# Kernel tuning notes

Measured on AMD Instinct MI355X. Metric: run time of the kernel, lower is better.

Reference implementation:

```python
import jax, jax.numpy as jnp
import numpy as np

B, S, E, H = 2, 2048, 1024, 16
D = E // H          # head_dim = 64
HK = H // 4         # heads per kernel group = 4
MASKED_BIAS = -10000.0


def _dwconv_causal(x, w, b):
    # x: [B, h, S, D], w: [D, k], b: [D]; causal depthwise conv along S
    k = w.shape[1]
    s = x.shape[2]
    xp = jnp.pad(x, ((0, 0), (0, 0), (k - 1, 0), (0, 0)))
    out = b
    for i in range(k):
        out = out + xp[:, :, i:i + s, :] * w[:, i]
    return out


def setup_inputs() -> dict:
    key = jax.random.key(0)
    ks = jax.random.split(key, 32)
    inp = {
        'hidden_states': jax.random.normal(ks[0], (B, S, E), jnp.float32),
        'c_attn_w': jax.random.normal(ks[1], (E, 3 * E), jnp.float32) * 0.02,
        'c_attn_b': jnp.zeros((3 * E,), jnp.float32),
        'c_proj_w': jax.random.normal(ks[2], (E, E), jnp.float32) * 0.02,
        'c_proj_b': jnp.zeros((E,), jnp.float32),
    }
    i = 3
    for pre in ('q', 'k', 'v'):
        for kern in (3, 5, 7):
            inp[f'{pre}w{kern}'] = jax.random.normal(ks[i], (D, kern), jnp.float32) * (1.0 / kern)
            inp[f'{pre}b{kern}'] = jnp.zeros((D,), jnp.float32)
            i += 1
    return inp


def _forward(hidden_states, c_attn_w, c_attn_b, c_proj_w, c_proj_b,
             qw3, qb3, qw5, qb5, qw7, qb7,
             kw3, kb3, kw5, kb5, kw7, kb7,
             vw3, vb3, vw5, vb5, vw7, vb7):
    qkv = hidden_states @ c_attn_w + c_attn_b            # [B,S,3E]
    q, k, v = jnp.split(qkv, 3, axis=-1)

    def split_heads(t):
        return t.reshape(B, S, H, D).transpose(0, 2, 1, 3)  # [B,H,S,D]

    q, k, v = split_heads(q), split_heads(k), split_heads(v)

    def tranception_mix(t, ws_bs):
        parts = [t[:, :HK]]
        for g, (w, b) in enumerate(ws_bs):
            parts.append(_dwconv_causal(t[:, (g + 1) * HK:(g + 2) * HK], w, b))
        return jnp.concatenate(parts, axis=1)

    q = tranception_mix(q, [(qw3, qb3), (qw5, qb5), (qw7, qb7)])
    k = tranception_mix(k, [(kw3, kb3), (kw5, kb5), (kw7, kb7)])
    v = tranception_mix(v, [(vw3, vb3), (vw5, vb5), (vw7, vb7)])

    scores = jnp.einsum('bhqd,bhkd->bhqk', q, k) / jnp.sqrt(jnp.float32(D))
    causal = jnp.tril(jnp.ones((S, S), bool))
    scores = jnp.where(causal, scores, jnp.float32(MASKED_BIAS))
    attn = jax.nn.softmax(scores, axis=-1)
    out = jnp.einsum('bhqk,bhkd->bhqd', attn, v)
    out = out.transpose(0, 2, 1, 3).reshape(B, S, E)
    return out @ c_proj_w + c_proj_b


def reference(hidden_states, c_attn_w, c_attn_b, c_proj_w, c_proj_b,
              qw3, qb3, qw5, qb5, qw7, qb7,
              kw3, kb3, kw5, kb5, kw7, kb7,
              vw3, vb3, vw5, vb5, vw7, vb7):
    return _forward(hidden_states, c_attn_w, c_attn_b, c_proj_w, c_proj_b,
                    qw3, qb3, qw5, qb5, qw7, qb7,
                    kw3, kb3, kw5, kb5, kw7, kb7,
                    vw3, vb3, vw5, vb5, vw7, vb7)
```

## Files before the change

kernel.cpp:

```cpp
#include <hip/hip_runtime.h>
#include <stdint.h>
#include <math.h>

typedef unsigned short u16;
typedef __attribute__((ext_vector_type(8))) short short8;
typedef __attribute__((ext_vector_type(4))) float floatx4;

#define DEV static __device__ __forceinline__

struct alignas(8) us4 { u16 x, y, z, w; };
struct alignas(16) us8 { u16 v[8]; };
struct alignas(16) f4 { float x, y, z, w; };
struct alignas(8) f2 { float x, y; };
struct alignas(8) u32x2 { uint32_t x, y; };

DEV u16 f2bf(float f) {
  uint32_t u = __float_as_uint(f);
  u += 0x7fffu + ((u >> 16) & 1u);
  return (u16)(u >> 16);
}
DEV float bf2f(u16 h) { return __uint_as_float(((uint32_t)h) << 16); }

DEV uint32_t pkbf(float a, float b) {
#if __has_builtin(__builtin_amdgcn_cvt_pk_bf16_f32)
  typedef __attribute__((ext_vector_type(2))) __bf16 bf2_t;
  bf2_t v = __builtin_amdgcn_cvt_pk_bf16_f32(a, b);
  uint32_t r; __builtin_memcpy(&r, &v, 4); return r;
#else
  return (uint32_t)f2bf(a) | ((uint32_t)f2bf(b) << 16);
#endif
}

DEV float fexp2(float x) {
#if __has_builtin(__builtin_amdgcn_exp2f)
  return __builtin_amdgcn_exp2f(x);
#else
  return exp2f(x);
#endif
}

DEV void load_lds16(const void* g, void* l) {
  __builtin_amdgcn_global_load_lds((const __attribute__((address_space(1))) void*)g,
                                   (__attribute__((address_space(3))) void*)l, 16, 0, 0);
}

__global__ __launch_bounds__(256) void prep_fused(const float* __restrict__ hidden, u16* __restrict__ h_bf,
                                                  const float* __restrict__ attn_w, u16* __restrict__ wqkvT,
                                                  const float* __restrict__ proj_w, u16* __restrict__ wprojT) {
  __shared__ float tile[32][33];
  const int bx = blockIdx.x;
  const int t = threadIdx.x;
  if (bx < 4096) {
    const int i = (bx * 256 + t) * 4;
    f4 v = *(const f4*)(hidden + i);
    us4 o; o.x = f2bf(v.x); o.y = f2bf(v.y); o.z = f2bf(v.z); o.w = f2bf(v.w);
    *(us4*)(h_bf + i) = o;
    return;
  }
  const float* in; u16* out; int K, N, n0, k0;
  if (bx < 7168) {
    const int bid = bx - 4096;
    in = attn_w; out = wqkvT; K = 1024; N = 3072;
    n0 = (bid % 96) * 32; k0 = (bid / 96) * 32;
  } else {
    const int bid = bx - 7168;
    in = proj_w; out = wprojT; K = 1024; N = 1024;
    n0 = (bid & 31) * 32; k0 = (bid >> 5) * 32;
  }
  const int tx = t & 31, ty = t >> 5;
  for (int i = ty; i < 32; i += 8)
    tile[i][tx] = in[(size_t)(k0 + i) * N + n0 + tx];
  __syncthreads();
  for (int i = ty; i < 32; i += 8)
    out[(size_t)(n0 + i) * K + k0 + tx] = f2bf(tile[tx][i]);
}

template <int EPI, int BN, int NGRP>
__global__ __launch_bounds__(256) void gemm_bt(const u16* __restrict__ A,
                                               const u16* __restrict__ Bt,
                                               const float* __restrict__ bias,
                                               void* __restrict__ outp,
                                               int M, int N, int K) {
  constexpr int NT = BN / 32;
  __shared__ u16 lA[128 * 64];
  __shared__ u16 lB[BN * 64];
  const int t = threadIdx.x;
  const int w = t >> 6, lane = t & 63;
  const int quad = lane >> 4, l15 = lane & 15;
  const int wm = w >> 1, wn = w & 1;
  const int wn_off = wn * (BN / 2);

  const int bid = blockIdx.x;
  const int gsz = 32 * NGRP;
  const int grp = bid / gsz;
  const int r = bid - grp * gsz;
  const int m0 = (r & 31) * 128;
  const int n0 = (grp * NGRP + (r >> 5)) * BN;

  floatx4 acc[4][NT] = {};

  const int srow = t >> 3;
  const int scol = (((t & 7) ^ (srow & 7)) << 3);
  const u16* gA = A + (size_t)(m0 + srow) * K + scol;
  const u16* gB = Bt + (size_t)(n0 + srow) * K + scol;
  u16* sA = lA + t * 8;
  u16* sB = lB + t * 8;
  const size_t rstep = (size_t)32 * K;

  for (int k0 = 0; k0 < K; k0 += 64) {
#pragma unroll
    for (int c = 0; c < 4; c++) load_lds16(gA + c * rstep, sA + c * 2048);
#pragma unroll
    for (int c = 0; c < BN / 32; c++) load_lds16(gB + c * rstep, sB + c * 2048);
    gA += 64; gB += 64;
    __syncthreads();
#pragma unroll
    for (int kc = 0; kc < 2; kc++) {
      short8 af[4], bfr[NT];
#pragma unroll
      for (int mt = 0; mt < 4; mt++)
        af[mt] = *(const short8*)&lA[(wm * 64 + mt * 16 + l15) * 64 + (((kc * 4 + quad) ^ (l15 & 7)) << 3)];
#pragma unroll
      for (int nt = 0; nt < NT; nt++)
        bfr[nt] = *(const short8*)&lB[(wn_off + nt * 16 + l15) * 64 + (((kc * 4 + quad) ^ (l15 & 7)) << 3)];
#pragma unroll
      for (int mt = 0; mt < 4; mt++)
#pragma unroll
        for (int nt = 0; nt < NT; nt++)
          acc[mt][nt] = __builtin_amdgcn_mfma_f32_16x16x32_bf16(bfr[nt], af[mt], acc[mt][nt], 0, 0, 0);
    }
    __syncthreads();
  }

  if (EPI == 0) {
    u16* outq = (u16*)outp;
#pragma unroll
    for (int nt = 0; nt < NT; nt++) {
      const int nb = n0 + wn_off + nt * 16 + quad * 4;
      const f4 bn4 = *(const f4*)&bias[nb];
      const int tensor = nb >> 10, e = nb & 1023;
      const int h = e >> 6, d = e & 63;
      const size_t abase = (size_t)tensor * 4194304 + (size_t)h * 131072 + d;
#pragma unroll
      for (int mt = 0; mt < 4; mt++) {
        const int rr = m0 + wm * 64 + mt * 16 + l15;
        const int b = rr >> 11, s = rr & 2047;
        u32x2 o;
        o.x = pkbf(acc[mt][nt][0] + bn4.x, acc[mt][nt][1] + bn4.y);
        o.y = pkbf(acc[mt][nt][2] + bn4.z, acc[mt][nt][3] + bn4.w);
        *(u32x2*)&outq[abase + (size_t)b * 2097152 + (size_t)s * 64] = o;
      }
    }
  } else {
    float* outf = (float*)outp;
#pragma unroll
    for (int nt = 0; nt < NT; nt++) {
      const int nb = n0 + wn_off + nt * 16 + quad * 4;
      const f4 bn4 = *(const f4*)&bias[nb];
#pragma unroll
      for (int mt = 0; mt < 4; mt++) {
        const int rr = m0 + wm * 64 + mt * 16 + l15;
        f4 o;
        o.x = acc[mt][nt][0] + bn4.x;
        o.y = acc[mt][nt][1] + bn4.y;
        o.z = acc[mt][nt][2] + bn4.z;
        o.w = acc[mt][nt][3] + bn4.w;
        *(f4*)&outf[(size_t)rr * N + nb] = o;
      }
    }
  }
}

struct ConvW { const float* w[9]; const float* b[9]; };

template <int K>
DEV void conv_run(const u16* xt, int sl0, int d, const float* wp, const float* bp,
                  float qscale, float* out32) {
  float wr[K];
#pragma unroll
  for (int j = 0; j < K; j++) wr[j] = wp[d * K + j];
  const float br = bp[d];
  float win[K];
#pragma unroll
  for (int m = 1; m < K; m++) win[m] = bf2f(xt[(sl0 + 6 - K + m) * 68 + d]);
#pragma unroll
  for (int i = 0; i < 32; i++) {
#pragma unroll
    for (int m = 0; m < K - 1; m++) win[m] = win[m + 1];
    win[K - 1] = bf2f(xt[(sl0 + 6 + i) * 68 + d]);
    float val = br;
#pragma unroll
    for (int j = 0; j < K; j++) val += wr[j] * win[j];
    out32[i] = val * qscale;
  }
}

__global__ __launch_bounds__(256) void conv_mix(const u16* __restrict__ qkv, ConvW cw,
                                                u16* __restrict__ qpost,
                                                u16* __restrict__ kpost,
                                                u16* __restrict__ vpostT) {
  __shared__ u16 xt[134 * 68];
  __shared__ u16 yt[64 * 136];
  const int t = threadIdx.x;
  const int s0 = blockIdx.x * 128;
  const int h = blockIdx.y;
  const int tz = blockIdx.z;
  const int tensor = tz >> 1, b = tz & 1;
  const u16* src = qkv + (((size_t)tensor * 2 + b) * 16 + h) * 131072;

  for (int idx = t; idx < 134 * 16; idx += 256) {
    const int row = idx >> 4, c4 = (idx & 15) << 2;
    const int s = s0 - 6 + row;
    us4 v = {0, 0, 0, 0};
    if (s >= 0) v = *(const us4*)&src[(size_t)s * 64 + c4];
    *(us4*)&xt[row * 68 + c4] = v;
  }
  __syncthreads();

  const int group = h >> 2;
  const float* wp = (group > 0) ? cw.w[tensor * 3 + group - 1] : nullptr;
  const float* bp = (group > 0) ? cw.b[tensor * 3 + group - 1] : nullptr;
  const float qscale = (tensor == 0) ? 0.18033688f : 1.0f;

  const int d = t & 63;
  const int sl0 = (t >> 6) * 32;

  float out32[32];
  if (group == 0) {
#pragma unroll
    for (int i = 0; i < 32; i++)
      out32[i] = bf2f(xt[(sl0 + 6 + i) * 68 + d]) * qscale;
  } else if (group == 1) {
    conv_run<3>(xt, sl0, d, wp, bp, qscale, out32);
  } else if (group == 2) {
    conv_run<5>(xt, sl0, d, wp, bp, qscale, out32);
  } else {
    conv_run<7>(xt, sl0, d, wp, bp, qscale, out32);
  }

  if (tensor < 2) {
    u16* outp = (tensor == 0) ? qpost : kpost;
    const size_t ob = (((size_t)b * 16 + h) * 2048 + s0) * 64;
#pragma unroll
    for (int i = 0; i < 32; i++)
      outp[ob + (size_t)(sl0 + i) * 64 + d] = f2bf(out32[i]);
  } else {
#pragma unroll
    for (int i = 0; i < 32; i++)
      yt[d * 136 + sl0 + i] = f2bf(out32[i]);
    __syncthreads();
    const size_t ob = ((size_t)b * 16 + h) * 64;
    const int sl = (t & 15) * 8;
#pragma unroll
    for (int pass = 0; pass < 4; pass++) {
      const int dd = (t >> 4) + pass * 16;
      us8 vv = *(const us8*)&yt[dd * 136 + sl];
      *(us8*)&vpostT[(ob + dd) * 2048 + s0 + sl] = vv;
    }
  }
}

__global__ __launch_bounds__(256) void attn_fwd(const u16* __restrict__ Q,
                                                const u16* __restrict__ Kp,
                                                const u16* __restrict__ Vt,
                                                u16* __restrict__ Out) {
  __shared__ u16 lK[2][128 * 64];
  __shared__ u16 lV[2][64 * 128];
  __shared__ u16 lP[4][32 * 64];
  const int t = threadIdx.x;
  const int w = t >> 6, lane = t & 63;
  const int quad = lane >> 4, l15 = lane & 15;
  const int e7 = l15 & 7;

  const int lin = blockIdx.x;
  const int xcd = lin & 7;
  const int s = lin >> 3;
  const int grp = s & 3;
  const int qsel = s >> 2;
  const int bh = grp * 8 + xcd;
  const int qi = (qsel < 8) ? qsel : 23 - qsel;

  const int b = bh >> 4, h = bh & 15;
  const size_t qkbase = (size_t)bh * 131072;
  const int qblk = qi * 128 + w * 32;

  const int krow = t >> 3;
  const int kcol = (((t & 7) ^ (krow & 7)) << 3);
  const u16* gK = Kp + qkbase + (size_t)krow * 64 + kcol;
  const int vrow = t >> 4;
  const int vcol = (((t & 15) ^ vrow) << 3);
  const u16* gV = Vt + qkbase + (size_t)vrow * 2048 + vcol;
  u16* myP = lP[w];

  short8 qf[2][2];
#pragma unroll
  for (int qt = 0; qt < 2; qt++)
#pragma unroll
    for (int kc = 0; kc < 2; kc++)
      qf[qt][kc] = *(const short8*)&Q[qkbase + (size_t)(qblk + qt * 16 + l15) * 64 + kc * 32 + quad * 8];

  {
    u16* sK = &lK[0][0] + t * 8;
    u16* sV = &lV[0][0] + t * 8;
#pragma unroll
    for (int c = 0; c < 4; c++) {
      load_lds16(gK + (size_t)(c * 32) * 64, sK + c * 2048);
      load_lds16(gV + c * 16 * 2048, sV + c * 2048);
    }
  }
  asm volatile("s_waitcnt vmcnt(0)" ::: "memory");
  __builtin_amdgcn_s_barrier();

  float lst[2] = {0.0f, 0.0f};
  floatx4 accO[4][2] = {};

  for (int j = 0; j <= qi; ++j) {
    const int cur = j & 1;

    if (j < qi) {
      const int j0n = (j + 1) * 128;
      u16* sK = &lK[cur ^ 1][0] + t * 8;
      u16* sV = &lV[cur ^ 1][0] + t * 8;
#pragma unroll
      for (int c = 0; c < 4; c++) {
        load_lds16(gK + (size_t)(j0n + c * 32) * 64, sK + c * 2048);
        load_lds16(gV + j0n + c * 16 * 2048, sV + c * 2048);
      }
    }

    const int j0 = j * 128;
    const u16* cK = lK[cur];
    const u16* cV = lV[cur];

    floatx4 accS[8][2] = {};
    __builtin_amdgcn_s_setprio(1);
#pragma unroll
    for (int kvt = 0; kvt < 8; kvt++) {
#pragma unroll
      for (int kc = 0; kc < 2; kc++) {
        const short8 a = *(const short8*)&cK[(kvt * 16 + l15) * 64 + (((kc * 4 + quad) ^ e7) << 3)];
#pragma unroll
        for (int qt = 0; qt < 2; qt++)
          accS[kvt][qt] = __builtin_amdgcn_mfma_f32_16x16x32_bf16(a, qf[qt][kc], accS[kvt][qt], 0, 0, 0);
      }
    }
    __builtin_amdgcn_s_setprio(0);

    if (j == qi) {
#pragma unroll
      for (int qt = 0; qt < 2; qt++) {
        const int q = qblk + qt * 16 + l15;
#pragma unroll
        for (int kvt = 0; kvt < 8; kvt++)
#pragma unroll
          for (int r = 0; r < 4; r++) {
            const int kv = j0 + kvt * 16 + quad * 4 + r;
            if (kv > q) accS[kvt][qt][r] = -3.0e38f;
          }
      }
    }

    uint32_t pk01[2][8], pk23[2][8];
#pragma unroll
    for (int qt = 0; qt < 2; qt++) {
      float ts = 0.0f;
#pragma unroll
      for (int kvt = 0; kvt < 8; kvt++) {
        const float p0 = fexp2(accS[kvt][qt][0]);
        const float p1 = fexp2(accS[kvt][qt][1]);
        const float p2 = fexp2(accS[kvt][qt][2]);
        const float p3 = fexp2(accS[kvt][qt][3]);
        ts += (p0 + p1) + (p2 + p3);
        pk01[qt][kvt] = pkbf(p0, p1);
        pk23[qt][kvt] = pkbf(p2, p3);
      }
      lst[qt] += ts;
    }

#pragma unroll
    for (int kvh = 0; kvh < 2; kvh++) {
#pragma unroll
      for (int qt = 0; qt < 2; qt++) {
        const int prow = (qt * 16 + l15) * 64;
#pragma unroll
        for (int kt = 0; kt < 4; kt++) {
          const int kvt = kvh * 4 + kt;
          const int slot = (kt * 2 + (quad >> 1)) ^ e7;
          u32x2 pk; pk.x = pk01[qt][kvt]; pk.y = pk23[qt][kvt];
          *(u32x2*)&myP[prow + slot * 8 + (quad & 1) * 4] = pk;
        }
      }
      asm volatile("s_waitcnt lgkmcnt(0)" ::: "memory");
      __builtin_amdgcn_s_setprio(1);
#pragma unroll
      for (int kk = 0; kk < 2; kk++) {
        const int kvc = kvh * 2 + kk;
        short8 pf[2];
#pragma unroll
        for (int qt = 0; qt < 2; qt++)
          pf[qt] = *(const short8*)&myP[(qt * 16 + l15) * 64 + (((kk * 4 + quad) ^ e7) << 3)];
#pragma unroll
        for (int dt = 0; dt < 4; dt++) {
          const short8 vf = *(const short8*)&cV[(dt * 16 + l15) * 128 + (((kvc * 4 + quad) ^ l15) << 3)];
#pragma unroll
          for (int qt = 0; qt < 2; qt++)
            accO[dt][qt] = __builtin_amdgcn_mfma_f32_16x16x32_bf16(vf, pf[qt], accO[dt][qt], 0, 0, 0);
        }
      }
      __builtin_amdgcn_s_setprio(0);
    }

    if (j < qi) {
      asm volatile("s_waitcnt vmcnt(0)" ::: "memory");
      __builtin_amdgcn_s_barrier();
    }
  }

#pragma unroll
  for (int qt = 0; qt < 2; qt++) {
    lst[qt] += __shfl_xor(lst[qt], 16);
    lst[qt] += __shfl_xor(lst[qt], 32);
  }

#pragma unroll
  for (int qt = 0; qt < 2; qt++) {
    const float inv = 1.0f / lst[qt];
    const int q = qblk + qt * 16 + l15;
#pragma unroll
    for (int dt = 0; dt < 4; dt++) {
      u32x2 o;
      o.x = pkbf(accO[dt][qt][0] * inv, accO[dt][qt][1] * inv);
      o.y = pkbf(accO[dt][qt][2] * inv, accO[dt][qt][3] * inv);
      *(u32x2*)&Out[((size_t)b * 2048 + q) * 1024 + h * 64 + dt * 16 + quad * 4] = o;
    }
  }
}

extern "C" void kernel_launch(void* const* d_in, const int* in_sizes, int n_in,
                              void* d_out, int out_size, void* d_ws, size_t ws_size,
                              hipStream_t stream) {
  (void)in_sizes; (void)n_in; (void)out_size; (void)ws_size;
  const float* hidden = (const float*)d_in[0];
  const float* attn_w = (const float*)d_in[1];
  const float* attn_b = (const float*)d_in[2];
  const float* proj_w = (const float*)d_in[3];
  const float* proj_b = (const float*)d_in[4];
  ConvW cw;
  for (int i = 0; i < 9; i++) {
    cw.w[i] = (const float*)d_in[5 + 2 * i];
    cw.b[i] = (const float*)d_in[6 + 2 * i];
  }

  uint8_t* ws = (uint8_t*)d_ws;
  u16* h_bf   = (u16*)(ws + 0);
  u16* wqkvT  = (u16*)(ws + 8388608);
  u16* qkvpre = (u16*)(ws + 14680064);
  u16* qpost  = (u16*)(ws + 39845888);
  u16* kpost  = (u16*)(ws + 48234496);
  u16* vpostT = (u16*)(ws + 56623104);
  u16* attno  = (u16*)(ws + 65011712);
  u16* wprojT = (u16*)(ws + 73400320);

  prep_fused<<<8192, 256, 0, stream>>>(hidden, h_bf, attn_w, wqkvT, proj_w, wprojT);
  gemm_bt<0, 128, 6><<<768, 256, 0, stream>>>(h_bf, wqkvT, attn_b, (void*)qkvpre, 4096, 3072, 1024);
  conv_mix<<<dim3(16, 16, 6), 256, 0, stream>>>(qkvpre, cw, qpost, kpost, vpostT);
  attn_fwd<<<dim3(512), 256, 0, stream>>>(qpost, kpost, vpostT, attno);
  gemm_bt<1, 64, 8><<<512, 256, 0, stream>>>(attno, wprojT, proj_b, d_out, 4096, 1024, 1024);
}
```

Baseline: 240.5 us.

## Split long causal query blocks across two KV halves with a reduce kernel

Query blocks 8-15 now have their KV range split into two halves, each handled by a separate workgroup that writes unnormalised bf16 partial outputs and row sums. A new attn_reduce kernel sums the two halves and normalises. A reorder table schedules long and short work items. The aim is to balance per-block work and shorten the causal tail, at the cost of an extra launch, partial-buffer traffic and bf16 rounding of the partials.

```diff
diff --git a/kernel.cpp b/kernel.cpp
--- a/kernel.cpp
+++ b/kernel.cpp
@@ -260,10 +260,17 @@
   }
 }
 
+static __device__ const unsigned char kOrder[24] = {
+  7, 8, 10, 12, 14, 16, 18, 20, 22, 23,
+  6, 21, 5, 19, 4, 17, 3, 15, 2, 13, 1, 11, 0, 9
+};
+
 __global__ __launch_bounds__(256) void attn_fwd(const u16* __restrict__ Q,
                                                 const u16* __restrict__ Kp,
                                                 const u16* __restrict__ Vt,
-                                                u16* __restrict__ Out) {
+                                                u16* __restrict__ Out,
+                                                u16* __restrict__ Opart,
+                                                float* __restrict__ lpart) {
   __shared__ u16 lK[2][128 * 64];
   __shared__ u16 lV[2][64 * 128];
   __shared__ u16 lP[4][32 * 64];
@@ -274,11 +281,19 @@
 
   const int lin = blockIdx.x;
   const int xcd = lin & 7;
-  const int s = lin >> 3;
-  const int grp = s & 3;
-  const int qsel = s >> 2;
+  const int rest = lin >> 3;
+  const int grp = rest / 24;
+  const int slot = kOrder[rest - grp * 24];
   const int bh = grp * 8 + xcd;
-  const int qi = (qsel < 8) ? qsel : 23 - qsel;
+
+  int qi, jbeg, jend, split, half;
+  if (slot < 8) {
+    qi = slot; jbeg = 0; jend = qi + 1; split = 0; half = 0;
+  } else {
+    const int k = slot - 8;
+    qi = 8 + (k >> 1); half = k & 1;
+    jbeg = half ? 8 : 0; jend = half ? qi + 1 : 8; split = 1;
+  }
 
   const int b = bh >> 4, h = bh & 15;
   const size_t qkbase = (size_t)bh * 131072;
@@ -300,12 +315,13 @@
       qf[qt][kc] = *(const short8*)&Q[qkbase + (size_t)(qblk + qt * 16 + l15) * 64 + kc * 32 + quad * 8];
 
   {
+    const int j0 = jbeg * 128;
     u16* sK = &lK[0][0] + t * 8;
     u16* sV = &lV[0][0] + t * 8;
 #pragma unroll
     for (int c = 0; c < 4; c++) {
-      load_lds16(gK + (size_t)(c * 32) * 64, sK + c * 2048);
-      load_lds16(gV + c * 16 * 2048, sV + c * 2048);
+      load_lds16(gK + (size_t)(j0 + c * 32) * 64, sK + c * 2048);
+      load_lds16(gV + j0 + c * 16 * 2048, sV + c * 2048);
     }
   }
   asm volatile("s_waitcnt vmcnt(0)" ::: "memory");
@@ -314,10 +330,10 @@
   float lst[2] = {0.0f, 0.0f};
   floatx4 accO[4][2] = {};
 
-  for (int j = 0; j <= qi; ++j) {
-    const int cur = j & 1;
-
-    if (j < qi) {
+  for (int j = jbeg; j < jend; ++j) {
+    const int cur = (j - jbeg) & 1;
+
+    if (j + 1 < jend) {
       const int j0n = (j + 1) * 128;
       u16* sK = &lK[cur ^ 1][0] + t * 8;
       u16* sV = &lV[cur ^ 1][0] + t * 8;
@@ -385,9 +401,9 @@
 #pragma unroll
         for (int kt = 0; kt < 4; kt++) {
           const int kvt = kvh * 4 + kt;
-          const int slot = (kt * 2 + (quad >> 1)) ^ e7;
+          const int slotp = (kt * 2 + (quad >> 1)) ^ e7;
           u32x2 pk; pk.x = pk01[qt][kvt]; pk.y = pk23[qt][kvt];
-          *(u32x2*)&myP[prow + slot * 8 + (quad & 1) * 4] = pk;
+          *(u32x2*)&myP[prow + slotp * 8 + (quad & 1) * 4] = pk;
         }
       }
       asm volatile("s_waitcnt lgkmcnt(0)" ::: "memory");
@@ -410,7 +426,7 @@
       __builtin_amdgcn_s_setprio(0);
     }
 
-    if (j < qi) {
+    if (j + 1 < jend) {
       asm volatile("s_waitcnt vmcnt(0)" ::: "memory");
       __builtin_amdgcn_s_barrier();
     }
@@ -422,17 +438,69 @@
     lst[qt] += __shfl_xor(lst[qt], 32);
   }
 
-#pragma unroll
-  for (int qt = 0; qt < 2; qt++) {
-    const float inv = 1.0f / lst[qt];
-    const int q = qblk + qt * 16 + l15;
-#pragma unroll
-    for (int dt = 0; dt < 4; dt++) {
-      u32x2 o;
-      o.x = pkbf(accO[dt][qt][0] * inv, accO[dt][qt][1] * inv);
-      o.y = pkbf(accO[dt][qt][2] * inv, accO[dt][qt][3] * inv);
-      *(u32x2*)&Out[((size_t)b * 2048 + q) * 1024 + h * 64 + dt * 16 + quad * 4] = o;
-    }
+  if (!split) {
+#pragma unroll
+    for (int qt = 0; qt < 2; qt++) {
+      const float inv = 1.0f / lst[qt];
+      const int q = qblk + qt * 16 + l15;
+#pragma unroll
+      for (int dt = 0; dt < 4; dt++) {
+        u32x2 o;
+        o.x = pkbf(accO[dt][qt][0] * inv, accO[dt][qt][1] * inv);
+        o.y = pkbf(accO[dt][qt][2] * inv, accO[dt][qt][3] * inv);
+        *(u32x2*)&Out[((size_t)b * 2048 + q) * 1024 + h * 64 + dt * 16 + quad * 4] = o;
+      }
+    }
+  } else {
+    const int pidx = (bh * 8 + (qi - 8)) * 2 + half;
+    u16* op = Opart + (size_t)pidx * 8192;
+#pragma unroll
+    for (int qt = 0; qt < 2; qt++) {
+      const int ql = w * 32 + qt * 16 + l15;
+#pragma unroll
+      for (int dt = 0; dt < 4; dt++) {
+        u32x2 o;
+        o.x = pkbf(accO[dt][qt][0], accO[dt][qt][1]);
+        o.y = pkbf(accO[dt][qt][2], accO[dt][qt][3]);
+        *(u32x2*)&op[(size_t)ql * 64 + dt * 16 + quad * 4] = o;
+      }
+      if (quad == 0) lpart[pidx * 128 + ql] = lst[qt];
+    }
+  }
+}
+
+__global__ __launch_bounds__(256) void attn_reduce(const u16* __restrict__ Opart,
+                                                   const float* __restrict__ lpart,
+                                                   u16* __restrict__ Out) {
+  const int qr = blockIdx.x;
+  const int bh = blockIdx.y;
+  const int b = bh >> 4, h = bh & 15;
+  const int t = threadIdx.x;
+  const int row = t >> 1, dh = (t & 1) * 32;
+  const int pbase = (bh * 8 + qr) * 2;
+
+  const float l1 = lpart[pbase * 128 + row];
+  const float l2 = lpart[(pbase + 1) * 128 + row];
+  const float inv = 1.0f / (l1 + l2);
+
+  const u16* s1 = Opart + ((size_t)pbase * 128 + row) * 64 + dh;
+  const u16* s2 = Opart + ((size_t)(pbase + 1) * 128 + row) * 64 + dh;
+  u16* dst = Out + ((size_t)b * 2048 + (8 + qr) * 128 + row) * 1024 + h * 64 + dh;
+#pragma unroll
+  for (int i = 0; i < 4; i++) {
+    us8 v1 = *(const us8*)&s1[i * 8];
+    us8 v2 = *(const us8*)&s2[i * 8];
+    float o[8];
+#pragma unroll
+    for (int e = 0; e < 8; e++) o[e] = (bf2f(v1.v[e]) + bf2f(v2.v[e])) * inv;
+    us4 a, c;
+    uint32_t w0 = pkbf(o[0], o[1]), w1 = pkbf(o[2], o[3]);
+    uint32_t w2 = pkbf(o[4], o[5]), w3 = pkbf(o[6], o[7]);
+    u32x2 lo; lo.x = w0; lo.y = w1;
+    u32x2 hi; hi.x = w2; hi.y = w3;
+    *(u32x2*)&dst[i * 8] = lo;
+    *(u32x2*)&dst[i * 8 + 4] = hi;
+    (void)a; (void)c;
   }
 }
 
@@ -460,10 +528,13 @@
   u16* vpostT = (u16*)(ws + 56623104);
   u16* attno  = (u16*)(ws + 65011712);
   u16* wprojT = (u16*)(ws + 73400320);
+  u16* Opart  = (u16*)(ws + 0);
+  float* lpart = (float*)(ws + 8388608);
 
   prep_fused<<<8192, 256, 0, stream>>>(hidden, h_bf, attn_w, wqkvT, proj_w, wprojT);
   gemm_bt<0, 128, 6><<<768, 256, 0, stream>>>(h_bf, wqkvT, attn_b, (void*)qkvpre, 4096, 3072, 1024);
   conv_mix<<<dim3(16, 16, 6), 256, 0, stream>>>(qkvpre, cw, qpost, kpost, vpostT);
-  attn_fwd<<<dim3(512), 256, 0, stream>>>(qpost, kpost, vpostT, attno);
+  attn_fwd<<<dim3(768), 256, 0, stream>>>(qpost, kpost, vpostT, attno, Opart, lpart);
+  attn_reduce<<<dim3(8, 32), 256, 0, stream>>>(Opart, lpart, attno);
   gemm_bt<1, 64, 8><<<512, 256, 0, stream>>>(attno, wprojT, proj_b, d_out, 4096, 1024, 1024);
 }
```

New measurement: 242.7 us. Within noise of the previous version (+0.9%).
